# Performance work log

Measured on AMD Instinct MI355X. Metric: run time of the kernel, lower is better.

## Reference

```python
import jax, jax.numpy as jnp
import numpy as np

CHANNEL = 200
NEIGH = 8
OUT_C = CHANNEL - NEIGH + 1  # 193 sliding channel windows


def setup_inputs() -> dict:
    key = jax.random.key(0)
    k_x, k_w, k_b = jax.random.split(key, 3)
    x = jax.random.normal(k_x, (16, CHANNEL, 128, 128), dtype=jnp.float32)
    # Per-window 1x1 conv params: weight[o, k] maps input channel o+k -> output channel o.
    # Matches PyTorch Conv2d default init (kaiming_uniform with fan_in = NEIGH).
    bound = 1.0 / np.sqrt(NEIGH)
    W = jax.random.uniform(k_w, (OUT_C, NEIGH), minval=-bound, maxval=bound, dtype=jnp.float32)
    b = jax.random.uniform(k_b, (OUT_C,), minval=-bound, maxval=bound, dtype=jnp.float32)
    return {"x": x, "W": W, "b": b}


def reference(x, W, b):
    # Fused sliding-window channel mix: out[b,o,h,w] = sum_k W[o,k] * x[b,o+k,h,w] + b[o]
    # Loop is over the small fixed NEIGH (8), not over data dims; avoids materializing
    # the [B, OUT_C, NEIGH, H, W] window tensor.
    out_c = x.shape[1] - NEIGH + 1
    out = b[None, :, None, None]
    for k in range(NEIGH):
        out = out + W[None, :, k, None, None] * x[:, k:k + out_c]
    return out
```

## Files before the change

kernel.cpp:

```cpp
#include <hip/hip_runtime.h>

#define CH    200
#define NE    8
#define OUTC  (CH - NE + 1)
#define HW    (128 * 128)
#define VEC   4
#define THREADS 256
#define NCHUNKS 4


typedef float f32x4 __attribute__((ext_vector_type(4)));

__device__ __forceinline__ void fma4(float4& a, float s, const float4& v) {
  a.x += s * v.x; a.y += s * v.y; a.z += s * v.z; a.w += s * v.w;
}

__global__ __launch_bounds__(THREADS, 4) void neigh_conv_kernel(
    const float* __restrict__ x, const float* __restrict__ W,
    const float* __restrict__ b, float* __restrict__ out) {
  __shared__ __align__(16) float sW[OUTC * NE];
  __shared__ float sb[OUTC];
  for (int i = threadIdx.x; i < OUTC * NE; i += THREADS) sW[i] = W[i];
  for (int i = threadIdx.x; i < OUTC; i += THREADS) sb[i] = b[i];
  __syncthreads();

  const int pos   = (blockIdx.x * THREADS + threadIdx.x) * VEC;
  const int n     = blockIdx.y;
  const int chunk = blockIdx.z;
  const int c0 = (chunk * OUTC) / NCHUNKS;
  const int c1 = ((chunk + 1) * OUTC) / NCHUNKS;

  const float* xp = x + (size_t)n * CH * HW + pos;
  float* op       = out + (size_t)n * OUTC * HW + pos;

  float4 win[NE - 1];
#pragma unroll
  for (int k = 0; k < NE - 1; ++k)
    win[k] = *(const float4*)(xp + (size_t)(c0 + k) * HW);
  float4 p0 = *(const float4*)(xp + (size_t)(c0 + NE - 1) * HW);
  float4 p1 = *(const float4*)(xp + (size_t)min(c0 + NE, CH - 1) * HW);

  for (int c = c0; c < c1; ++c) {
    const float4 cur = p0;
    p0 = p1;
    const int cnext = min(c + NE + 1, CH - 1);
    p1 = *(const float4*)(xp + (size_t)cnext * HW);

    const float4 w0 = *(const float4*)&sW[c * NE];
    const float4 w1 = *(const float4*)&sW[c * NE + 4];
    const float bb  = sb[c];
    float4 acc = make_float4(bb, bb, bb, bb);
    fma4(acc, w0.x, win[0]);
    fma4(acc, w0.y, win[1]);
    fma4(acc, w0.z, win[2]);
    fma4(acc, w0.w, win[3]);
    fma4(acc, w1.x, win[4]);
    fma4(acc, w1.y, win[5]);
    fma4(acc, w1.z, win[6]);
    fma4(acc, w1.w, cur);
    f32x4 accv;
    accv.x = acc.x; accv.y = acc.y; accv.z = acc.z; accv.w = acc.w;
    __builtin_nontemporal_store(accv, (f32x4*)(op + (size_t)c * HW));

#pragma unroll
    for (int k = 0; k < NE - 2; ++k) win[k] = win[k + 1];
    win[NE - 2] = cur;
  }
}

extern "C" void kernel_launch(void* const* d_in, const int* in_sizes, int n_in,
                              void* d_out, int out_size, void* d_ws, size_t ws_size,
                              hipStream_t stream) {
  const float* x = (const float*)d_in[0];
  const float* W = (const float*)d_in[1];
  const float* b = (const float*)d_in[2];
  float* out = (float*)d_out;

  const int N = 16;

  dim3 grid(HW / VEC / THREADS , N, NCHUNKS);
  neigh_conv_kernel<<<grid, THREADS, 0, stream>>>(x, W, b, out);
}
```

Baseline: 361.7 us.

## Software-pipeline channel loads in 8-channel groups with triple register buffers

```diff
diff --git a/kernel.cpp b/kernel.cpp
--- a/kernel.cpp
+++ b/kernel.cpp
@@ -7,15 +7,16 @@
 #define VEC   4
 #define THREADS 256
 #define NCHUNKS 4
+#define NGROUPS 6
 
 
 typedef float f32x4 __attribute__((ext_vector_type(4)));
 
-__device__ __forceinline__ void fma4(float4& a, float s, const float4& v) {
-  a.x += s * v.x; a.y += s * v.y; a.z += s * v.z; a.w += s * v.w;
+__device__ __forceinline__ void fma4(f32x4& a, float s, f32x4 v) {
+  a[0] += s * v[0]; a[1] += s * v[1]; a[2] += s * v[2]; a[3] += s * v[3];
 }
 
-__global__ __launch_bounds__(THREADS, 4) void neigh_conv_kernel(
+__global__ __launch_bounds__(THREADS) void neigh_conv_kernel(
     const float* __restrict__ x, const float* __restrict__ W,
     const float* __restrict__ b, float* __restrict__ out) {
   __shared__ __align__(16) float sW[OUTC * NE];
@@ -33,38 +34,55 @@
   const float* xp = x + (size_t)n * CH * HW + pos;
   float* op       = out + (size_t)n * OUTC * HW + pos;
 
-  float4 win[NE - 1];
+  f32x4 A[8], B[8], C[8];
 #pragma unroll
-  for (int k = 0; k < NE - 1; ++k)
-    win[k] = *(const float4*)(xp + (size_t)(c0 + k) * HW);
-  float4 p0 = *(const float4*)(xp + (size_t)(c0 + NE - 1) * HW);
-  float4 p1 = *(const float4*)(xp + (size_t)min(c0 + NE, CH - 1) * HW);
+  for (int k = 0; k < 8; ++k)
+    A[k] = *(const f32x4*)(xp + (size_t)(c0 + k) * HW);
+#pragma unroll
+  for (int k = 0; k < 8; ++k)
+    B[k] = *(const f32x4*)(xp + (size_t)(c0 + 8 + k) * HW);
 
-  for (int c = c0; c < c1; ++c) {
-    const float4 cur = p0;
-    p0 = p1;
-    const int cnext = min(c + NE + 1, CH - 1);
-    p1 = *(const float4*)(xp + (size_t)cnext * HW);
+  int c = c0;
+#pragma unroll 1
+  for (int g = 0; g < NGROUPS; ++g, c += 8) {
+#pragma unroll
+    for (int k = 0; k < 8; ++k) {
+      const int ch = min(c + 16 + k, CH - 1);
+      C[k] = *(const f32x4*)(xp + (size_t)ch * HW);
+    }
+#pragma unroll
+    for (int j = 0; j < 8; ++j) {
+      const int cc = c + j;
+      const f32x4 w0 = *(const f32x4*)&sW[cc * NE];
+      const f32x4 w1 = *(const f32x4*)&sW[cc * NE + 4];
+      const float bb = sb[cc];
+      f32x4 acc = {bb, bb, bb, bb};
+#pragma unroll
+      for (int k = 0; k < 8; ++k) {
+        const int idx = j + k;
+        const f32x4 v = (idx < 8) ? A[idx & 7] : B[idx & 7];
+        const float w = (k < 4) ? w0[k] : w1[k - 4];
+        fma4(acc, w, v);
+      }
+      __builtin_nontemporal_store(acc, (f32x4*)(op + (size_t)cc * HW));
+    }
+#pragma unroll
+    for (int k = 0; k < 8; ++k) A[k] = B[k];
+#pragma unroll
+    for (int k = 0; k < 8; ++k) B[k] = C[k];
+  }
 
-    const float4 w0 = *(const float4*)&sW[c * NE];
-    const float4 w1 = *(const float4*)&sW[c * NE + 4];
-    const float bb  = sb[c];
-    float4 acc = make_float4(bb, bb, bb, bb);
-    fma4(acc, w0.x, win[0]);
-    fma4(acc, w0.y, win[1]);
-    fma4(acc, w0.z, win[2]);
-    fma4(acc, w0.w, win[3]);
-    fma4(acc, w1.x, win[4]);
-    fma4(acc, w1.y, win[5]);
-    fma4(acc, w1.z, win[6]);
-    fma4(acc, w1.w, cur);
-    f32x4 accv;
-    accv.x = acc.x; accv.y = acc.y; accv.z = acc.z; accv.w = acc.w;
-    __builtin_nontemporal_store(accv, (f32x4*)(op + (size_t)c * HW));
-
+  if (c < c1) {
+    const f32x4 w0 = *(const f32x4*)&sW[c * NE];
+    const f32x4 w1 = *(const f32x4*)&sW[c * NE + 4];
+    const float bb = sb[c];
+    f32x4 acc = {bb, bb, bb, bb};
 #pragma unroll
-    for (int k = 0; k < NE - 2; ++k) win[k] = win[k + 1];
-    win[NE - 2] = cur;
+    for (int k = 0; k < 8; ++k) {
+      const float w = (k < 4) ? w0[k] : w1[k - 4];
+      fma4(acc, w, A[k]);
+    }
+    __builtin_nontemporal_store(acc, (f32x4*)(op + (size_t)c * HW));
   }
 }
 
```

New measurement: 351.7 us. -2.8%, faster.
